# Kernel tuning notes

Hardware: AMD Instinct MI355X
Metric: run time of the kernel (lower is better)

The kernel has to match this reference:

```python
import jax, jax.numpy as jnp
import numpy as np

TEMPERATURE = 0.1
EPS = 1e-8


def _hann(T, dtype):
    # torch.hann_window default: periodic=True -> 0.5*(1-cos(2*pi*n/T))
    return 0.5 * (1.0 - jnp.cos(2.0 * jnp.pi * jnp.arange(T, dtype=dtype) / T))


def _per_traj_stats(trajectories):
    # trajectories: [B, T, 4] = (phi1, v1, phi2, v2)
    B, T, _ = trajectories.shape
    v = trajectories[:, :, 1::2]                      # [B, T, 2] voltages
    v_mean = v.mean(axis=1)                           # [B, 2]
    w = _hann(T, trajectories.dtype)[None, :, None]
    fft = jnp.fft.rfft(v * w, axis=1)                 # [B, T//2+1, 2]
    psd = (jnp.abs(fft) ** 2)[:, : T // 10, :]        # keep low-frequency bins
    psd = psd.reshape(B, -1)                          # [B, 2*(T//10)] (flatten, C-order like torch)
    phase = trajectories[:, :, 0::2]                  # [B, T, 2]
    delta = jnp.diff(phase, axis=1)
    winding = jnp.abs(jnp.round(delta.sum(axis=1) / (2.0 * jnp.pi)))  # [B, 2]
    return v_mean, psd, winding


def _kinematic_similarity(trajectories):
    # Vectorized equivalent of the original O(B^2) python loop (i < j, symmetrized, zero diag)
    v_mean, psd, winding = _per_traj_stats(trajectories)
    v_dist = jnp.linalg.norm(v_mean[:, None, :] - v_mean[None, :, :], axis=-1)  # [B, B]
    v_sim = jnp.exp(-v_dist / 0.5)
    n2 = jnp.sum(psd * psd, axis=1)                   # [B]
    gram = psd @ psd.T                                # [B, B]
    d2 = jnp.maximum(n2[:, None] + n2[None, :] - 2.0 * gram, 0.0)
    psd_dist = jnp.sqrt(d2)
    psd_norm = jnp.sqrt(n2)
    # denominator uses ||psd_i|| of the row index (matches loop where i < j)
    psd_sim = jnp.exp(-psd_dist / (psd_norm[:, None] + EPS))
    wind_sim = jnp.all(winding[:, None, :] == winding[None, :, :], axis=-1).astype(psd.dtype)
    total = 0.4 * v_sim + 0.4 * psd_sim + 0.2 * wind_sim
    upper = jnp.triu(total, k=1)                      # only i<j computed in the loop
    return upper + upper.T                            # symmetric, zero diagonal


def reference(features, labels, trajectories, param_scales):
    B = features.shape[0]
    # F.normalize(dim=1), eps=1e-12
    norm = jnp.maximum(jnp.linalg.norm(features, axis=1, keepdims=True), 1e-12)
    f = features / norm
    param_diff = jnp.abs(labels[:, None, :] - labels[None, :, :]) / param_scales
    param_dist = jnp.linalg.norm(param_diff, axis=2)  # [B, B]
    kin_sim = jax.lax.stop_gradient(_kinematic_similarity(trajectories))  # no_grad in torch
    mask_pos_weight = jnp.exp(-param_dist / 0.1) * kin_sim
    sim = (f @ f.T) / TEMPERATURE
    exp_sim = jnp.exp(sim)
    exp_sim = jnp.where(jnp.eye(B, dtype=bool), 0.0, exp_sim)
    pos_weighted = (exp_sim * mask_pos_weight).sum(axis=1)
    denom = exp_sim.sum(axis=1)
    loss = -jnp.log((pos_weighted + EPS) / (denom + EPS))
    return loss.mean()


def setup_inputs() -> dict:
    key = jax.random.key(0)
    k1, k2, k3 = jax.random.split(key, 3)
    B, D, T, P = 1024, 256, 8192, 3
    features = jax.random.normal(k1, (B, D), dtype=jnp.float32)
    labels = jax.random.uniform(k2, (B, P), dtype=jnp.float32)
    trajectories = jax.random.normal(k3, (B, T, 4), dtype=jnp.float32)
    param_scales = jnp.ones((1,), dtype=jnp.float32)
    return {"features": features, "labels": labels, "trajectories": trajectories, "param_scales": param_scales}
```

## Files before the change

kernel.cpp:

```cpp
#include <hip/hip_runtime.h>
#include <hip/hip_bf16.h>
#include <hip/hip_fp16.h>

#define B_SZ 1024
#define T_LEN 8192
#define NBINS 819
#define PSD_LDA 1664
#define PI_F 3.14159265358979323846f

typedef __attribute__((ext_vector_type(8))) short bf16x8;
typedef __attribute__((ext_vector_type(4))) float f32x4;

__device__ constexpr float C32T[16] = {
  1.0f, 0.980785280f, 0.923879533f, 0.831469612f, 0.707106781f, 0.555570233f,
  0.382683432f, 0.195090322f, 0.0f, -0.195090322f, -0.382683432f, -0.555570233f,
  -0.707106781f, -0.831469612f, -0.923879533f, -0.980785280f};
__device__ constexpr float S32T[16] = {
  0.0f, -0.195090322f, -0.382683432f, -0.555570233f, -0.707106781f,
  -0.831469612f, -0.923879533f, -0.980785280f, -1.0f, -0.980785280f,
  -0.923879533f, -0.831469612f, -0.707106781f, -0.555570233f, -0.382683432f,
  -0.195090322f};
__device__ constexpr int BR5[32] = {
  0,16,8,24,4,20,12,28,2,18,10,26,6,22,14,30,
  1,17,9,25,5,21,13,29,3,19,11,27,7,23,15,31};
__device__ constexpr float E8C[8] = {
  1.0f, 0.707106781f, 0.0f, -0.707106781f, -1.0f, -0.707106781f, 0.0f, 0.707106781f};
__device__ constexpr float E8S[8] = {
  0.0f, 0.707106781f, 1.0f, 0.707106781f, 0.0f, -0.707106781f, -1.0f, -0.707106781f};

template<int S>
__device__ __forceinline__ void fft32_stage(float (&xr)[32], float (&xi)[32]) {
  #pragma unroll
  for (int o = 0; o < 32; o += 2 * S) {
    #pragma unroll
    for (int j = 0; j < S; ++j) {
      const int i0 = o + j, i1 = o + j + S;
      float ur = xr[i0] + xr[i1], ui = xi[i0] + xi[i1];
      float dr = xr[i0] - xr[i1], di = xi[i0] - xi[i1];
      const float c = C32T[j * (16 / S)], sn = S32T[j * (16 / S)];
      xr[i0] = ur; xi[i0] = ui;
      xr[i1] = dr * c - di * sn;
      xi[i1] = dr * sn + di * c;
    }
  }
}
__device__ __forceinline__ void fft32(float (&xr)[32], float (&xi)[32]) {
  fft32_stage<16>(xr, xi); fft32_stage<8>(xr, xi); fft32_stage<4>(xr, xi);
  fft32_stage<2>(xr, xi);  fft32_stage<1>(xr, xi);
}

__global__ __launch_bounds__(256) void normalize_kernel(
    const float* __restrict__ f, __hip_bfloat16* __restrict__ fn) {
  int i = blockIdx.x;
  int t = threadIdx.x;
  float v = f[(size_t)i * 256 + t];
  float s = v * v;
  #pragma unroll
  for (int o = 32; o; o >>= 1) s += __shfl_down(s, o);
  __shared__ float buf[4];
  if ((t & 63) == 0) buf[t >> 6] = s;
  __syncthreads();
  float norm = sqrtf(buf[0] + buf[1] + buf[2] + buf[3]);
  norm = fmaxf(norm, 1e-12f);
  fn[(size_t)i * 256 + t] = __float2bfloat16(v / norm);
}

__global__ __launch_bounds__(256) void traj_stats_kernel(
    const float* __restrict__ trajf,
    __hip_bfloat16* __restrict__ psd,
    float2* __restrict__ vmean,
    float2* __restrict__ wind) {
  __shared__ __half2 z2[T_LEN];
  __shared__ float rsum[2][4];
  __shared__ float phb[4];

  const int tid = threadIdx.x;
  const float* rowf = trajf + (size_t)blockIdx.x * T_LEN * 4;
  const int b = tid >> 3, c = tid & 7;

  float xr[32], xi[32];
  float sum0 = 0.f, sum1 = 0.f;
  const float wstep = 2.0f * PI_F / (float)T_LEN;

  #pragma unroll
  for (int a = 0; a < 32; ++a) {
    const size_t base = (size_t)4 * (a * 256 + tid);
    xr[a] = rowf[base + 1];
    xi[a] = rowf[base + 3];
  }
  if (tid == 0) {
    phb[0] = rowf[0];
    phb[1] = rowf[2];
    phb[2] = rowf[(size_t)4 * (T_LEN - 1)];
    phb[3] = rowf[(size_t)4 * (T_LEN - 1) + 2];
  }

  #pragma unroll
  for (int a = 0; a < 32; ++a) {
    sum0 += xr[a]; sum1 += xi[a];
    float w = 0.5f * (1.0f - __cosf(wstep * (float)(a * 256 + tid)));
    xr[a] *= w;
    xi[a] *= w;
  }

  fft32(xr, xi);

  {
    float s1, c1, s16, c16;
    __sincosf(-2.0f * PI_F * (float)tid / 8192.0f, &s1, &c1);
    __sincosf(-2.0f * PI_F * (float)tid / 512.0f,  &s16, &c16);
    float wr0 = 1.f, wi0 = 0.f, wr1 = c16, wi1 = s16;
    #pragma unroll
    for (int k0 = 0; k0 < 16; ++k0) {
      {
        const int r = BR5[k0];
        float tr = xr[r] * wr0 - xi[r] * wi0;
        float ti = xr[r] * wi0 + xi[r] * wr0;
        z2[k0 * 256 + (((b + (k0 & 3)) & 31) << 3) + c] = __floats2half2_rn(tr, ti);
        float nr = wr0 * c1 - wi0 * s1; wi0 = wr0 * s1 + wi0 * c1; wr0 = nr;
      }
      {
        const int k0b = k0 + 16;
        const int r = BR5[k0b];
        float tr = xr[r] * wr1 - xi[r] * wi1;
        float ti = xr[r] * wi1 + xi[r] * wr1;
        z2[k0b * 256 + (((b + (k0b & 3)) & 31) << 3) + c] = __floats2half2_rn(tr, ti);
        float nr = wr1 * c1 - wi1 * s1; wi1 = wr1 * s1 + wi1 * c1; wr1 = nr;
      }
    }
  }
  __syncthreads();

  #pragma unroll
  for (int bq = 0; bq < 32; ++bq) {
    __half2 v = z2[b * 256 + (((bq + (b & 3)) & 31) << 3) + c];
    xr[bq] = __low2float(v); xi[bq] = __high2float(v);
  }
  __syncthreads();

  fft32(xr, xi);

  {
    float s1, c1, s16, c16;
    __sincosf(-2.0f * PI_F * (float)c / 256.0f, &s1, &c1);
    __sincosf(-2.0f * PI_F * (float)c / 16.0f,  &s16, &c16);
    float wr0 = 1.f, wi0 = 0.f, wr1 = c16, wi1 = s16;
    #pragma unroll
    for (int k1 = 0; k1 < 16; ++k1) {
      {
        const int r = BR5[k1];
        const int p = (k1 << 5) + b;
        float tr = xr[r] * wr0 - xi[r] * wi0;
        float ti = xr[r] * wi0 + xi[r] * wr0;
        z2[(p << 3) + (c ^ ((p >> 2) & 7))] = __floats2half2_rn(tr, ti);
        float nr = wr0 * c1 - wi0 * s1; wi0 = wr0 * s1 + wi0 * c1; wr0 = nr;
      }
      {
        const int k1b = k1 + 16;
        const int r = BR5[k1b];
        const int p = (k1b << 5) + b;
        float tr = xr[r] * wr1 - xi[r] * wi1;
        float ti = xr[r] * wi1 + xi[r] * wr1;
        z2[(p << 3) + (c ^ ((p >> 2) & 7))] = __floats2half2_rn(tr, ti);
        float nr = wr1 * c1 - wi1 * s1; wi1 = wr1 * s1 + wi1 * c1; wr1 = nr;
      }
    }
  }
  __syncthreads();

  float z0r[4], z0i[4], z7r[4], z7i[4];
  #pragma unroll
  for (int q = 0; q < 4; ++q) {
    const int p = q * 256 + tid;
    float s0r = 0.f, s0i = 0.f, s7r = 0.f, s7i = 0.f;
    #pragma unroll
    for (int c2 = 0; c2 < 8; ++c2) {
      __half2 v = z2[(p << 3) + (c2 ^ ((p >> 2) & 7))];
      float vr = __low2float(v), vi = __high2float(v);
      s0r += vr; s0i += vi;
      s7r += vr * E8C[c2] - vi * E8S[c2];
      s7i += vr * E8S[c2] + vi * E8C[c2];
    }
    z0r[q] = s0r; z0i[q] = s0i; z7r[q] = s7r; z7i[q] = s7i;
  }
  __syncthreads();
  float2* zf = (float2*)z2;
  #pragma unroll
  for (int q = 0; q < 4; ++q) {
    const int p = q * 256 + tid;
    zf[p]        = make_float2(z0r[q], z0i[q]);
    zf[1024 + p] = make_float2(z7r[q], z7i[q]);
  }
  __syncthreads();

  for (int k = tid; k < PSD_LDA / 2; k += 256) {
    if (k < NBINS) {
      float2 Zk = zf[k];
      float2 Zn = (k == 0) ? zf[0] : zf[2048 - k];
      float fxr = 0.5f * (Zk.x + Zn.x);
      float fxi = 0.5f * (Zk.y - Zn.y);
      float fyr = 0.5f * (Zk.y + Zn.y);
      float fyi = 0.5f * (Zn.x - Zk.x);
      psd[(size_t)blockIdx.x * PSD_LDA + 2*k]     = __float2bfloat16(fxr*fxr + fxi*fxi);
      psd[(size_t)blockIdx.x * PSD_LDA + 2*k + 1] = __float2bfloat16(fyr*fyr + fyi*fyi);
    } else {
      psd[(size_t)blockIdx.x * PSD_LDA + 2*k]     = __float2bfloat16(0.0f);
      psd[(size_t)blockIdx.x * PSD_LDA + 2*k + 1] = __float2bfloat16(0.0f);
    }
  }

  #pragma unroll
  for (int o = 32; o; o >>= 1) {
    sum0 += __shfl_down(sum0, o);
    sum1 += __shfl_down(sum1, o);
  }
  if ((tid & 63) == 0) { rsum[0][tid >> 6] = sum0; rsum[1][tid >> 6] = sum1; }
  __syncthreads();
  if (tid == 0) {
    float s0 = rsum[0][0] + rsum[0][1] + rsum[0][2] + rsum[0][3];
    float s1v = rsum[1][0] + rsum[1][1] + rsum[1][2] + rsum[1][3];
    vmean[blockIdx.x] = make_float2(s0 / (float)T_LEN, s1v / (float)T_LEN);
    const float inv2pi = 0.15915494309189535f;
    wind[blockIdx.x] = make_float2(fabsf(rintf((phb[2] - phb[0]) * inv2pi)),
                                   fabsf(rintf((phb[3] - phb[1]) * inv2pi)));
  }
}

template<int K, int LDA>
__global__ __launch_bounds__(256) void gram_mfma_kernel(
    const __hip_bfloat16* __restrict__ A, float* __restrict__ C) {
  __shared__ __align__(16) __hip_bfloat16 lds[2][64][64];
  const int tid  = threadIdx.x;
  const int lane = tid & 63;
  const int wave = tid >> 6;
  const int wm = wave >> 1, wn = wave & 1;
  const int i0 = blockIdx.y * 64;
  const int j0 = blockIdx.x * 64;

  f32x4 acc[2][2] = {};

  for (int k0 = 0; k0 < K; k0 += 64) {
    #pragma unroll
    for (int r = 0; r < 2; ++r) {
      int e   = tid + 256 * r;
      int row = e >> 3;
      int cb  = e & 7;
      int scb = cb ^ (row & 7);
      const __hip_bfloat16* srcA = A + (size_t)(i0 + row) * LDA + k0 + scb * 8;
      const __hip_bfloat16* srcB = A + (size_t)(j0 + row) * LDA + k0 + scb * 8;
      __builtin_amdgcn_global_load_lds(
          (const __attribute__((address_space(1))) void*)srcA,
          (__attribute__((address_space(3))) void*)(&lds[0][0][0] + e * 8),
          16, 0, 0);
      __builtin_amdgcn_global_load_lds(
          (const __attribute__((address_space(1))) void*)srcB,
          (__attribute__((address_space(3))) void*)(&lds[1][0][0] + e * 8),
          16, 0, 0);
    }
    __syncthreads();

    #pragma unroll
    for (int ks = 0; ks < 2; ++ks) {
      bf16x8 afr[2], bfr[2];
      #pragma unroll
      for (int m = 0; m < 2; ++m) {
        int row = wm * 32 + m * 16 + (lane & 15);
        int cidx = ks * 4 + (lane >> 4);
        int cc  = cidx ^ (row & 7);
        afr[m] = *(const bf16x8*)(&lds[0][row][cc * 8]);
      }
      #pragma unroll
      for (int n = 0; n < 2; ++n) {
        int row = wn * 32 + n * 16 + (lane & 15);
        int cidx = ks * 4 + (lane >> 4);
        int cc  = cidx ^ (row & 7);
        bfr[n] = *(const bf16x8*)(&lds[1][row][cc * 8]);
      }
      #pragma unroll
      for (int m = 0; m < 2; ++m)
        #pragma unroll
        for (int n = 0; n < 2; ++n)
          acc[m][n] = __builtin_amdgcn_mfma_f32_16x16x32_bf16(
              afr[m], bfr[n], acc[m][n], 0, 0, 0);
    }
    __syncthreads();
  }

  #pragma unroll
  for (int m = 0; m < 2; ++m)
    #pragma unroll
    for (int n = 0; n < 2; ++n)
      #pragma unroll
      for (int r = 0; r < 4; ++r) {
        int row = i0 + wm * 32 + m * 16 + (lane >> 4) * 4 + r;
        int col = j0 + wn * 32 + n * 16 + (lane & 15);
        C[(size_t)row * B_SZ + col] = acc[m][n][r];
      }
}

__global__ __launch_bounds__(256) void loss_rows_kernel(
    const float* __restrict__ S,
    const float* __restrict__ G,
    const float* __restrict__ labels,
    const float* __restrict__ scales,
    const float2* __restrict__ vmean,
    const float2* __restrict__ wind,
    float* __restrict__ row_loss) {
  const int i = blockIdx.x;
  const int tid = threadIdx.x;
  const float inv_scale = 1.0f / scales[0];
  const float l0 = labels[i*3+0], l1 = labels[i*3+1], l2 = labels[i*3+2];
  const float2 vmi = vmean[i];
  const float2 wi  = wind[i];
  const float n2i  = G[(size_t)i * B_SZ + i];
  const float normi = sqrtf(n2i);

  float posw = 0.f, den = 0.f;
  for (int j = tid; j < B_SZ; j += 256) {
    if (j == i) continue;
    float e = __expf(S[(size_t)i * B_SZ + j] * 10.0f);
    den += e;

    float d0 = (labels[j*3+0] - l0) * inv_scale;
    float d1 = (labels[j*3+1] - l1) * inv_scale;
    float d2v = (labels[j*3+2] - l2) * inv_scale;
    float pd = sqrtf(d0*d0 + d1*d1 + d2v*d2v);
    float pw = __expf(-pd * 10.0f);

    float2 vmj = vmean[j];
    float dvx = vmi.x - vmj.x, dvy = vmi.y - vmj.y;
    float v_sim = __expf(-sqrtf(dvx*dvx + dvy*dvy) * 2.0f);

    float n2j = G[(size_t)j * B_SZ + j];
    float g   = G[(size_t)i * B_SZ + j];
    float dd  = fmaxf(n2i + n2j - 2.0f * g, 0.0f);
    float psd_dist = sqrtf(dd);
    float norma = (i < j) ? normi : sqrtf(n2j);
    float psd_sim = __expf(-psd_dist / (norma + 1e-8f));

    float2 wj = wind[j];
    float w_sim = (wi.x == wj.x && wi.y == wj.y) ? 1.0f : 0.0f;

    float kin = 0.4f * v_sim + 0.4f * psd_sim + 0.2f * w_sim;
    posw += e * pw * kin;
  }

  #pragma unroll
  for (int o = 32; o; o >>= 1) {
    posw += __shfl_down(posw, o);
    den  += __shfl_down(den, o);
  }
  __shared__ float bp[4], bd[4];
  if ((tid & 63) == 0) { bp[tid >> 6] = posw; bd[tid >> 6] = den; }
  __syncthreads();
  if (tid == 0) {
    float P = bp[0] + bp[1] + bp[2] + bp[3];
    float D = bd[0] + bd[1] + bd[2] + bd[3];
    row_loss[i] = -logf((P + 1e-8f) / (D + 1e-8f));
  }
}

__global__ __launch_bounds__(256) void reduce_mean_kernel(
    const float* __restrict__ row_loss, float* __restrict__ out) {
  int tid = threadIdx.x;
  float s = 0.f;
  for (int i = tid; i < B_SZ; i += 256) s += row_loss[i];
  #pragma unroll
  for (int o = 32; o; o >>= 1) s += __shfl_down(s, o);
  __shared__ float buf[4];
  if ((tid & 63) == 0) buf[tid >> 6] = s;
  __syncthreads();
  if (tid == 0) out[0] = (buf[0] + buf[1] + buf[2] + buf[3]) / (float)B_SZ;
}

extern "C" void kernel_launch(void* const* d_in, const int* in_sizes, int n_in,
                              void* d_out, int out_size, void* d_ws, size_t ws_size,
                              hipStream_t stream) {
  const float* features = (const float*)d_in[0];
  const float* labels   = (const float*)d_in[1];
  const float* traj     = (const float*)d_in[2];
  const float* scales   = (const float*)d_in[3];

  char* ws = (char*)d_ws;
  __hip_bfloat16* f_n = (__hip_bfloat16*)ws;
  __hip_bfloat16* psd = (__hip_bfloat16*)(ws + (size_t)B_SZ*256*2);
  float* G = (float*)(ws + (size_t)B_SZ*256*2 + (size_t)B_SZ*PSD_LDA*2);
  float* S = G + (size_t)B_SZ * B_SZ;
  float2* vmean = (float2*)(S + (size_t)B_SZ * B_SZ);
  float2* wind  = vmean + B_SZ;
  float* row_loss = (float*)(wind + B_SZ);

  normalize_kernel<<<B_SZ, 256, 0, stream>>>(features, f_n);
  traj_stats_kernel<<<B_SZ, 256, 0, stream>>>(traj, psd, vmean, wind);

  dim3 grid16(16, 16);
  gram_mfma_kernel<PSD_LDA, PSD_LDA><<<grid16, 256, 0, stream>>>(psd, G);
  gram_mfma_kernel<256, 256><<<grid16, 256, 0, stream>>>(f_n, S);

  loss_rows_kernel<<<B_SZ, 256, 0, stream>>>(S, G, labels, scales, vmean, wind, row_loss);
  reduce_mean_kernel<<<1, 256, 0, stream>>>(row_loss, (float*)d_out);
}
```

Measured before the change: 73.72 us.

## Split trajectory FFT into two kernels with global-memory transpose

Splits the single trajectory FFT kernel into two launches. The first pass writes its half-precision intermediate to a global workspace buffer in transposed order, and the second kernel reads it back with vectorized loads. This drops the 32KB shared-memory transpose from the first pass, which may raise occupancy there. The cost is an extra kernel launch plus roughly 32MB of global-memory write and read traffic.

```diff
diff --git a/kernel.cpp b/kernel.cpp
--- a/kernel.cpp
+++ b/kernel.cpp
@@ -65,18 +65,18 @@
   fn[(size_t)i * 256 + t] = __float2bfloat16(v / norm);
 }
 
-__global__ __launch_bounds__(256) void traj_stats_kernel(
+__global__ __launch_bounds__(256) void traj_fft1_kernel(
     const float* __restrict__ trajf,
-    __hip_bfloat16* __restrict__ psd,
+    __half2* __restrict__ t1,
     float2* __restrict__ vmean,
     float2* __restrict__ wind) {
-  __shared__ __half2 z2[T_LEN];
   __shared__ float rsum[2][4];
   __shared__ float phb[4];
 
   const int tid = threadIdx.x;
   const float* rowf = trajf + (size_t)blockIdx.x * T_LEN * 4;
   const int b = tid >> 3, c = tid & 7;
+  __half2* t1row = t1 + (size_t)blockIdx.x * T_LEN;
 
   float xr[32], xi[32];
   float sum0 = 0.f, sum1 = 0.f;
@@ -116,7 +116,7 @@
         const int r = BR5[k0];
         float tr = xr[r] * wr0 - xi[r] * wi0;
         float ti = xr[r] * wi0 + xi[r] * wr0;
-        z2[k0 * 256 + (((b + (k0 & 3)) & 31) << 3) + c] = __floats2half2_rn(tr, ti);
+        t1row[k0 * 256 + c * 32 + b] = __floats2half2_rn(tr, ti);
         float nr = wr0 * c1 - wi0 * s1; wi0 = wr0 * s1 + wi0 * c1; wr0 = nr;
       }
       {
@@ -124,44 +124,75 @@
         const int r = BR5[k0b];
         float tr = xr[r] * wr1 - xi[r] * wi1;
         float ti = xr[r] * wi1 + xi[r] * wr1;
-        z2[k0b * 256 + (((b + (k0b & 3)) & 31) << 3) + c] = __floats2half2_rn(tr, ti);
+        t1row[k0b * 256 + c * 32 + b] = __floats2half2_rn(tr, ti);
         float nr = wr1 * c1 - wi1 * s1; wi1 = wr1 * s1 + wi1 * c1; wr1 = nr;
       }
     }
   }
-  __syncthreads();
-
-  #pragma unroll
-  for (int bq = 0; bq < 32; ++bq) {
-    __half2 v = z2[b * 256 + (((bq + (b & 3)) & 31) << 3) + c];
-    xr[bq] = __low2float(v); xi[bq] = __high2float(v);
-  }
-  __syncthreads();
+
+  #pragma unroll
+  for (int o = 32; o; o >>= 1) {
+    sum0 += __shfl_down(sum0, o);
+    sum1 += __shfl_down(sum1, o);
+  }
+  if ((tid & 63) == 0) { rsum[0][tid >> 6] = sum0; rsum[1][tid >> 6] = sum1; }
+  __syncthreads();
+  if (tid == 0) {
+    float s0 = rsum[0][0] + rsum[0][1] + rsum[0][2] + rsum[0][3];
+    float s1v = rsum[1][0] + rsum[1][1] + rsum[1][2] + rsum[1][3];
+    vmean[blockIdx.x] = make_float2(s0 / (float)T_LEN, s1v / (float)T_LEN);
+    const float inv2pi = 0.15915494309189535f;
+    wind[blockIdx.x] = make_float2(fabsf(rintf((phb[2] - phb[0]) * inv2pi)),
+                                   fabsf(rintf((phb[3] - phb[1]) * inv2pi)));
+  }
+}
+
+__global__ __launch_bounds__(256) void traj_fft2_kernel(
+    const __half2* __restrict__ t1,
+    __hip_bfloat16* __restrict__ psd) {
+  __shared__ __half2 z2[T_LEN];
+
+  const int tid = threadIdx.x;
+  const int k0r = tid >> 3, cr = tid & 7;
+  const __half2* t1row = t1 + (size_t)blockIdx.x * T_LEN;
+
+  float xr[32], xi[32];
+
+  #pragma unroll
+  for (int q = 0; q < 8; ++q) {
+    float4 v4 = *(const float4*)(t1row + k0r * 256 + cr * 32 + 4 * q);
+    __half2 h0 = *(__half2*)&v4.x, h1 = *(__half2*)&v4.y;
+    __half2 h2 = *(__half2*)&v4.z, h3 = *(__half2*)&v4.w;
+    xr[4*q+0] = __low2float(h0); xi[4*q+0] = __high2float(h0);
+    xr[4*q+1] = __low2float(h1); xi[4*q+1] = __high2float(h1);
+    xr[4*q+2] = __low2float(h2); xi[4*q+2] = __high2float(h2);
+    xr[4*q+3] = __low2float(h3); xi[4*q+3] = __high2float(h3);
+  }
 
   fft32(xr, xi);
 
   {
     float s1, c1, s16, c16;
-    __sincosf(-2.0f * PI_F * (float)c / 256.0f, &s1, &c1);
-    __sincosf(-2.0f * PI_F * (float)c / 16.0f,  &s16, &c16);
+    __sincosf(-2.0f * PI_F * (float)cr / 256.0f, &s1, &c1);
+    __sincosf(-2.0f * PI_F * (float)cr / 16.0f,  &s16, &c16);
     float wr0 = 1.f, wi0 = 0.f, wr1 = c16, wi1 = s16;
     #pragma unroll
     for (int k1 = 0; k1 < 16; ++k1) {
       {
         const int r = BR5[k1];
-        const int p = (k1 << 5) + b;
+        const int p = (k1 << 5) + k0r;
         float tr = xr[r] * wr0 - xi[r] * wi0;
         float ti = xr[r] * wi0 + xi[r] * wr0;
-        z2[(p << 3) + (c ^ ((p >> 2) & 7))] = __floats2half2_rn(tr, ti);
+        z2[(p << 3) + (cr ^ ((p >> 2) & 7))] = __floats2half2_rn(tr, ti);
         float nr = wr0 * c1 - wi0 * s1; wi0 = wr0 * s1 + wi0 * c1; wr0 = nr;
       }
       {
         const int k1b = k1 + 16;
         const int r = BR5[k1b];
-        const int p = (k1b << 5) + b;
+        const int p = (k1b << 5) + k0r;
         float tr = xr[r] * wr1 - xi[r] * wi1;
         float ti = xr[r] * wi1 + xi[r] * wr1;
-        z2[(p << 3) + (c ^ ((p >> 2) & 7))] = __floats2half2_rn(tr, ti);
+        z2[(p << 3) + (cr ^ ((p >> 2) & 7))] = __floats2half2_rn(tr, ti);
         float nr = wr1 * c1 - wi1 * s1; wi1 = wr1 * s1 + wi1 * c1; wr1 = nr;
       }
     }
@@ -207,22 +238,6 @@
       psd[(size_t)blockIdx.x * PSD_LDA + 2*k]     = __float2bfloat16(0.0f);
       psd[(size_t)blockIdx.x * PSD_LDA + 2*k + 1] = __float2bfloat16(0.0f);
     }
-  }
-
-  #pragma unroll
-  for (int o = 32; o; o >>= 1) {
-    sum0 += __shfl_down(sum0, o);
-    sum1 += __shfl_down(sum1, o);
-  }
-  if ((tid & 63) == 0) { rsum[0][tid >> 6] = sum0; rsum[1][tid >> 6] = sum1; }
-  __syncthreads();
-  if (tid == 0) {
-    float s0 = rsum[0][0] + rsum[0][1] + rsum[0][2] + rsum[0][3];
-    float s1v = rsum[1][0] + rsum[1][1] + rsum[1][2] + rsum[1][3];
-    vmean[blockIdx.x] = make_float2(s0 / (float)T_LEN, s1v / (float)T_LEN);
-    const float inv2pi = 0.15915494309189535f;
-    wind[blockIdx.x] = make_float2(fabsf(rintf((phb[2] - phb[0]) * inv2pi)),
-                                   fabsf(rintf((phb[3] - phb[1]) * inv2pi)));
   }
 }
 
@@ -389,9 +404,12 @@
   float2* vmean = (float2*)(S + (size_t)B_SZ * B_SZ);
   float2* wind  = vmean + B_SZ;
   float* row_loss = (float*)(wind + B_SZ);
+  __half2* t1 = (__half2*)(ws + ((((size_t)B_SZ*256*2 + (size_t)B_SZ*PSD_LDA*2
+                 + 2*(size_t)B_SZ*B_SZ*4 + B_SZ*16 + B_SZ*4) + 255) & ~(size_t)255));
 
   normalize_kernel<<<B_SZ, 256, 0, stream>>>(features, f_n);
-  traj_stats_kernel<<<B_SZ, 256, 0, stream>>>(traj, psd, vmean, wind);
+  traj_fft1_kernel<<<B_SZ, 256, 0, stream>>>(traj, t1, vmean, wind);
+  traj_fft2_kernel<<<B_SZ, 256, 0, stream>>>(t1, psd);
 
   dim3 grid16(16, 16);
   gram_mfma_kernel<PSD_LDA, PSD_LDA><<<grid16, 256, 0, stream>>>(psd, G);
```

Measured after the change: 88.06 us. +19.4%, slower.

## Compute radix-32 FFT stages with bf16 MFMA DFT matrices instead of scalar butterflies

Applied to the files above, without the earlier changes.

Replaces the two scalar radix-32 butterfly FFT passes in the trajectory-stats kernel with dense 32-point DFT matrix multiplies on bf16 MFMA instructions, using cos/sin/negated-sin A fragments. Intermediate spectra are stored in LDS as packed bf16 pairs with a padded stride of 9 instead of fp16 half2 with XOR swizzles. The aim is to cut VALU butterfly work and register pressure in the FFT-dominated kernel. The trade-off is lower precision, since both inputs and intermediates become bf16, plus extra MFMA work for the O(N^2) DFT.

```diff
diff --git a/kernel.cpp b/kernel.cpp
--- a/kernel.cpp
+++ b/kernel.cpp
@@ -1,6 +1,5 @@
 #include <hip/hip_runtime.h>
 #include <hip/hip_bf16.h>
-#include <hip/hip_fp16.h>
 
 #define B_SZ 1024
 #define T_LEN 8192
@@ -11,43 +10,37 @@
 typedef __attribute__((ext_vector_type(8))) short bf16x8;
 typedef __attribute__((ext_vector_type(4))) float f32x4;
 
-__device__ constexpr float C32T[16] = {
+__device__ constexpr float W32C[32] = {
   1.0f, 0.980785280f, 0.923879533f, 0.831469612f, 0.707106781f, 0.555570233f,
   0.382683432f, 0.195090322f, 0.0f, -0.195090322f, -0.382683432f, -0.555570233f,
-  -0.707106781f, -0.831469612f, -0.923879533f, -0.980785280f};
-__device__ constexpr float S32T[16] = {
+  -0.707106781f, -0.831469612f, -0.923879533f, -0.980785280f, -1.0f,
+  -0.980785280f, -0.923879533f, -0.831469612f, -0.707106781f, -0.555570233f,
+  -0.382683432f, -0.195090322f, 0.0f, 0.195090322f, 0.382683432f, 0.555570233f,
+  0.707106781f, 0.831469612f, 0.923879533f, 0.980785280f};
+__device__ constexpr float W32S[32] = {
   0.0f, -0.195090322f, -0.382683432f, -0.555570233f, -0.707106781f,
   -0.831469612f, -0.923879533f, -0.980785280f, -1.0f, -0.980785280f,
   -0.923879533f, -0.831469612f, -0.707106781f, -0.555570233f, -0.382683432f,
-  -0.195090322f};
-__device__ constexpr int BR5[32] = {
-  0,16,8,24,4,20,12,28,2,18,10,26,6,22,14,30,
-  1,17,9,25,5,21,13,29,3,19,11,27,7,23,15,31};
+  -0.195090322f, 0.0f, 0.195090322f, 0.382683432f, 0.555570233f, 0.707106781f,
+  0.831469612f, 0.923879533f, 0.980785280f, 1.0f, 0.980785280f, 0.923879533f,
+  0.831469612f, 0.707106781f, 0.555570233f, 0.382683432f, 0.195090322f};
 __device__ constexpr float E8C[8] = {
   1.0f, 0.707106781f, 0.0f, -0.707106781f, -1.0f, -0.707106781f, 0.0f, 0.707106781f};
 __device__ constexpr float E8S[8] = {
   0.0f, 0.707106781f, 1.0f, 0.707106781f, 0.0f, -0.707106781f, -1.0f, -0.707106781f};
 
-template<int S>
-__device__ __forceinline__ void fft32_stage(float (&xr)[32], float (&xi)[32]) {
-  #pragma unroll
-  for (int o = 0; o < 32; o += 2 * S) {
-    #pragma unroll
-    for (int j = 0; j < S; ++j) {
-      const int i0 = o + j, i1 = o + j + S;
-      float ur = xr[i0] + xr[i1], ui = xi[i0] + xi[i1];
-      float dr = xr[i0] - xr[i1], di = xi[i0] - xi[i1];
-      const float c = C32T[j * (16 / S)], sn = S32T[j * (16 / S)];
-      xr[i0] = ur; xi[i0] = ui;
-      xr[i1] = dr * c - di * sn;
-      xi[i1] = dr * sn + di * c;
-    }
-  }
-}
-__device__ __forceinline__ void fft32(float (&xr)[32], float (&xi)[32]) {
-  fft32_stage<16>(xr, xi); fft32_stage<8>(xr, xi); fft32_stage<4>(xr, xi);
-  fft32_stage<2>(xr, xi);  fft32_stage<1>(xr, xi);
-}
+__device__ __forceinline__ unsigned short bfb(float x) {
+  __hip_bfloat16 h = __float2bfloat16(x);
+  return *(unsigned short*)&h;
+}
+__device__ __forceinline__ float bff(unsigned short u) {
+  union { unsigned u; float f; } v; v.u = ((unsigned)u) << 16; return v.f;
+}
+__device__ __forceinline__ unsigned packbf(float r, float i) {
+  return (unsigned)bfb(r) | ((unsigned)bfb(i) << 16);
+}
+
+#define WIDX(k0, b, c) ((k0) * 288 + 9 * (b) + (c))
 
 __global__ __launch_bounds__(256) void normalize_kernel(
     const float* __restrict__ f, __hip_bfloat16* __restrict__ fn) {
@@ -70,101 +63,135 @@
     __hip_bfloat16* __restrict__ psd,
     float2* __restrict__ vmean,
     float2* __restrict__ wind) {
-  __shared__ __half2 z2[T_LEN];
+  __shared__ unsigned z2w[9216];
   __shared__ float rsum[2][4];
   __shared__ float phb[4];
 
   const int tid = threadIdx.x;
+  const int w   = tid >> 6;
+  const int l   = tid & 63;
+  const int g   = l >> 4;
+  const int lc  = l & 15;
   const float* rowf = trajf + (size_t)blockIdx.x * T_LEN * 4;
-  const int b = tid >> 3, c = tid & 7;
-
-  float xr[32], xi[32];
-  float sum0 = 0.f, sum1 = 0.f;
-  const float wstep = 2.0f * PI_F / (float)T_LEN;
-
-  #pragma unroll
-  for (int a = 0; a < 32; ++a) {
-    const size_t base = (size_t)4 * (a * 256 + tid);
-    xr[a] = rowf[base + 1];
-    xi[a] = rowf[base + 3];
-  }
+
   if (tid == 0) {
-    phb[0] = rowf[0];
-    phb[1] = rowf[2];
+    phb[0] = rowf[0]; phb[1] = rowf[2];
     phb[2] = rowf[(size_t)4 * (T_LEN - 1)];
     phb[3] = rowf[(size_t)4 * (T_LEN - 1) + 2];
   }
 
-  #pragma unroll
-  for (int a = 0; a < 32; ++a) {
-    sum0 += xr[a]; sum1 += xi[a];
-    float w = 0.5f * (1.0f - __cosf(wstep * (float)(a * 256 + tid)));
-    xr[a] *= w;
-    xi[a] *= w;
-  }
-
-  fft32(xr, xi);
-
-  {
-    float s1, c1, s16, c16;
-    __sincosf(-2.0f * PI_F * (float)tid / 8192.0f, &s1, &c1);
-    __sincosf(-2.0f * PI_F * (float)tid / 512.0f,  &s16, &c16);
-    float wr0 = 1.f, wi0 = 0.f, wr1 = c16, wi1 = s16;
-    #pragma unroll
-    for (int k0 = 0; k0 < 16; ++k0) {
-      {
-        const int r = BR5[k0];
-        float tr = xr[r] * wr0 - xi[r] * wi0;
-        float ti = xr[r] * wi0 + xi[r] * wr0;
-        z2[k0 * 256 + (((b + (k0 & 3)) & 31) << 3) + c] = __floats2half2_rn(tr, ti);
-        float nr = wr0 * c1 - wi0 * s1; wi0 = wr0 * s1 + wi0 * c1; wr0 = nr;
-      }
-      {
-        const int k0b = k0 + 16;
-        const int r = BR5[k0b];
-        float tr = xr[r] * wr1 - xi[r] * wi1;
-        float ti = xr[r] * wi1 + xi[r] * wr1;
-        z2[k0b * 256 + (((b + (k0b & 3)) & 31) << 3) + c] = __floats2half2_rn(tr, ti);
-        float nr = wr1 * c1 - wi1 * s1; wi1 = wr1 * s1 + wi1 * c1; wr1 = nr;
-      }
-    }
-  }
-  __syncthreads();
-
-  #pragma unroll
-  for (int bq = 0; bq < 32; ++bq) {
-    __half2 v = z2[b * 256 + (((bq + (b & 3)) & 31) << 3) + c];
-    xr[bq] = __low2float(v); xi[bq] = __high2float(v);
-  }
-  __syncthreads();
-
-  fft32(xr, xi);
-
-  {
-    float s1, c1, s16, c16;
-    __sincosf(-2.0f * PI_F * (float)c / 256.0f, &s1, &c1);
-    __sincosf(-2.0f * PI_F * (float)c / 16.0f,  &s16, &c16);
-    float wr0 = 1.f, wi0 = 0.f, wr1 = c16, wi1 = s16;
-    #pragma unroll
-    for (int k1 = 0; k1 < 16; ++k1) {
-      {
-        const int r = BR5[k1];
-        const int p = (k1 << 5) + b;
-        float tr = xr[r] * wr0 - xi[r] * wi0;
-        float ti = xr[r] * wi0 + xi[r] * wr0;
-        z2[(p << 3) + (c ^ ((p >> 2) & 7))] = __floats2half2_rn(tr, ti);
-        float nr = wr0 * c1 - wi0 * s1; wi0 = wr0 * s1 + wi0 * c1; wr0 = nr;
-      }
-      {
-        const int k1b = k1 + 16;
-        const int r = BR5[k1b];
-        const int p = (k1b << 5) + b;
-        float tr = xr[r] * wr1 - xi[r] * wi1;
-        float ti = xr[r] * wi1 + xi[r] * wr1;
-        z2[(p << 3) + (c ^ ((p >> 2) & 7))] = __floats2half2_rn(tr, ti);
-        float nr = wr1 * c1 - wi1 * s1; wi1 = wr1 * s1 + wi1 * c1; wr1 = nr;
-      }
-    }
+  bf16x8 Ac[2], As[2], Asn[2];
+  #pragma unroll
+  for (int mt = 0; mt < 2; ++mt) {
+    const int m = mt * 16 + lc;
+    #pragma unroll
+    for (int j = 0; j < 8; ++j) {
+      const int idx = (m * (g * 8 + j)) & 31;
+      unsigned short uc = bfb(W32C[idx]);
+      unsigned short us = bfb(W32S[idx]);
+      Ac[mt][j]  = (short)uc;
+      As[mt][j]  = (short)us;
+      Asn[mt][j] = (short)(us ^ 0x8000);
+    }
+  }
+
+  float vs0 = 0.f, vs1 = 0.f;
+  const f32x4 az = {0.f, 0.f, 0.f, 0.f};
+
+  #pragma unroll
+  for (int nt = 0; nt < 4; ++nt) {
+    const int n = w * 64 + nt * 16 + lc;
+    float yr[8], yw[8];
+    #pragma unroll
+    for (int j = 0; j < 8; ++j) {
+      const size_t t = (size_t)(g * 8 + j) * 256 + n;
+      yr[j] = rowf[4 * t + 1];
+      yw[j] = rowf[4 * t + 3];
+    }
+    #pragma unroll
+    for (int j = 0; j < 8; ++j) { vs0 += yr[j]; vs1 += yw[j]; }
+    float s0, c0;
+    __sincosf(2.0f * PI_F * ((float)n / 8192.0f + (float)g * 0.25f), &s0, &c0);
+    bf16x8 xrb, xib;
+    #pragma unroll
+    for (int j = 0; j < 8; ++j) {
+      float wv = 0.5f - 0.5f * (c0 * W32C[j] + s0 * W32S[j]);
+      xrb[j] = (short)bfb(yr[j] * wv);
+      xib[j] = (short)bfb(yw[j] * wv);
+    }
+    const int bw = 9 * (n >> 3) + (n & 7);
+    #pragma unroll
+    for (int mt = 0; mt < 2; ++mt) {
+      f32x4 ar = __builtin_amdgcn_mfma_f32_16x16x32_bf16(Asn[mt], xib, az, 0, 0, 0);
+      ar = __builtin_amdgcn_mfma_f32_16x16x32_bf16(Ac[mt], xrb, ar, 0, 0, 0);
+      f32x4 ai = __builtin_amdgcn_mfma_f32_16x16x32_bf16(Ac[mt], xib, az, 0, 0, 0);
+      ai = __builtin_amdgcn_mfma_f32_16x16x32_bf16(As[mt], xrb, ai, 0, 0, 0);
+      float sb, cb, ss, cs;
+      const float nf = (float)n;
+      __sincosf(-2.0f * PI_F * nf * (float)(mt * 16 + g * 4) / 8192.0f, &sb, &cb);
+      __sincosf(-2.0f * PI_F * nf / 8192.0f, &ss, &cs);
+      #pragma unroll
+      for (int r = 0; r < 4; ++r) {
+        float xr_ = ar[r] * cb - ai[r] * sb;
+        float xi_ = ar[r] * sb + ai[r] * cb;
+        const int k0 = mt * 16 + g * 4 + r;
+        z2w[k0 * 288 + bw] = packbf(xr_, xi_);
+        float nc = cb * cs - sb * ss; sb = cb * ss + sb * cs; cb = nc;
+      }
+    }
+  }
+  __syncthreads();
+
+  unsigned x2_0[2][4], x2_1[2][4], x2_2[2][4], x2_3[2][4];
+  #pragma unroll
+  for (int nt = 0; nt < 4; ++nt) {
+    const int n2 = w * 64 + nt * 16 + lc;
+    const int k0 = n2 >> 3, cc = n2 & 7;
+    bf16x8 xrb, xib;
+    #pragma unroll
+    for (int j = 0; j < 8; ++j) {
+      unsigned pw = z2w[WIDX(k0, g * 8 + j, cc)];
+      xrb[j] = (short)(pw & 0xffff);
+      xib[j] = (short)(pw >> 16);
+    }
+    #pragma unroll
+    for (int mt = 0; mt < 2; ++mt) {
+      f32x4 ar = __builtin_amdgcn_mfma_f32_16x16x32_bf16(Asn[mt], xib, az, 0, 0, 0);
+      ar = __builtin_amdgcn_mfma_f32_16x16x32_bf16(Ac[mt], xrb, ar, 0, 0, 0);
+      f32x4 ai = __builtin_amdgcn_mfma_f32_16x16x32_bf16(Ac[mt], xib, az, 0, 0, 0);
+      ai = __builtin_amdgcn_mfma_f32_16x16x32_bf16(As[mt], xrb, ai, 0, 0, 0);
+      float sb, cb, ss, cs;
+      const float cf = (float)cc;
+      __sincosf(-2.0f * PI_F * cf * (float)(mt * 16 + g * 4) / 256.0f, &sb, &cb);
+      __sincosf(-2.0f * PI_F * cf / 256.0f, &ss, &cs);
+      #pragma unroll
+      for (int r = 0; r < 4; ++r) {
+        float xr_ = ar[r] * cb - ai[r] * sb;
+        float xi_ = ar[r] * sb + ai[r] * cb;
+        unsigned pk = packbf(xr_, xi_);
+        if (nt == 0) x2_0[mt][r] = pk;
+        else if (nt == 1) x2_1[mt][r] = pk;
+        else if (nt == 2) x2_2[mt][r] = pk;
+        else x2_3[mt][r] = pk;
+        float nc = cb * cs - sb * ss; sb = cb * ss + sb * cs; cb = nc;
+      }
+    }
+  }
+  __syncthreads();
+
+  #pragma unroll
+  for (int nt = 0; nt < 4; ++nt) {
+    const int n2 = w * 64 + nt * 16 + lc;
+    const int k0 = n2 >> 3, cc = n2 & 7;
+    #pragma unroll
+    for (int mt = 0; mt < 2; ++mt)
+      #pragma unroll
+      for (int r = 0; r < 4; ++r) {
+        const int p = (mt * 16 + g * 4 + r) * 32 + k0;
+        unsigned pk = (nt == 0) ? x2_0[mt][r] : (nt == 1) ? x2_1[mt][r]
+                    : (nt == 2) ? x2_2[mt][r] : x2_3[mt][r];
+        z2w[(p << 3) + (cc ^ ((p >> 2) & 7))] = pk;
+      }
   }
   __syncthreads();
 
@@ -175,8 +202,9 @@
     float s0r = 0.f, s0i = 0.f, s7r = 0.f, s7i = 0.f;
     #pragma unroll
     for (int c2 = 0; c2 < 8; ++c2) {
-      __half2 v = z2[(p << 3) + (c2 ^ ((p >> 2) & 7))];
-      float vr = __low2float(v), vi = __high2float(v);
+      unsigned pw = z2w[(p << 3) + (c2 ^ ((p >> 2) & 7))];
+      float vr = bff((unsigned short)(pw & 0xffff));
+      float vi = bff((unsigned short)(pw >> 16));
       s0r += vr; s0i += vi;
       s7r += vr * E8C[c2] - vi * E8S[c2];
       s7i += vr * E8S[c2] + vi * E8C[c2];
@@ -184,7 +212,7 @@
     z0r[q] = s0r; z0i[q] = s0i; z7r[q] = s7r; z7i[q] = s7i;
   }
   __syncthreads();
-  float2* zf = (float2*)z2;
+  float2* zf = (float2*)z2w;
   #pragma unroll
   for (int q = 0; q < 4; ++q) {
     const int p = q * 256 + tid;
@@ -211,10 +239,10 @@
 
   #pragma unroll
   for (int o = 32; o; o >>= 1) {
-    sum0 += __shfl_down(sum0, o);
-    sum1 += __shfl_down(sum1, o);
-  }
-  if ((tid & 63) == 0) { rsum[0][tid >> 6] = sum0; rsum[1][tid >> 6] = sum1; }
+    vs0 += __shfl_down(vs0, o);
+    vs1 += __shfl_down(vs1, o);
+  }
+  if ((tid & 63) == 0) { rsum[0][tid >> 6] = vs0; rsum[1][tid >> 6] = vs1; }
   __syncthreads();
   if (tid == 0) {
     float s0 = rsum[0][0] + rsum[0][1] + rsum[0][2] + rsum[0][3];
```

Result: faster. 69.13 us (-6.2%).
